# Performance work log

Measured on AMD Instinct MI355X. Metric: run time of the kernel, lower is better.

## Reference

```python
import jax, jax.numpy as jnp
import numpy as np

H, DK = 8, 64
INNER = H * DK  # 512


def rel_shift(x):
    # Transformer-XL relative shift (NeMo style): pad left, reshape, drop first row.
    b, h, q, p = x.shape
    x = jnp.pad(x, ((0, 0), (0, 0), (0, 0), (1, 0)))
    x = x.reshape(b, h, p + 1, q)[:, :, 1:]
    return x.reshape(b, h, q, p)


def setup_inputs() -> dict:
    key = jax.random.key(0)
    ks = jax.random.split(key, 16)
    B, T, D = 8, 1024, 512
    s_d = 1.0 / np.sqrt(D)
    s_i = 1.0 / np.sqrt(INNER)
    return {
        "x": jax.random.normal(ks[0], (B, T, D), jnp.float32),
        "pos_emb": jax.random.normal(ks[1], (1, 2 * T - 1, INNER), jnp.float32),
        "w_qkv": jax.random.normal(ks[2], (D, 3 * INNER), jnp.float32) * s_d,
        "w_q": jax.random.normal(ks[3], (INNER, INNER), jnp.float32) * s_i,
        "b_q": jnp.zeros((INNER,), jnp.float32),
        "w_k": jax.random.normal(ks[4], (INNER, INNER), jnp.float32) * s_i,
        "b_k": jnp.zeros((INNER,), jnp.float32),
        "w_v": jax.random.normal(ks[5], (INNER, INNER), jnp.float32) * s_i,
        "b_v": jnp.zeros((INNER,), jnp.float32),
        "w_pos": jax.random.normal(ks[6], (INNER, INNER), jnp.float32) * s_i,
        "bias_u": jax.random.normal(ks[7], (H, DK), jnp.float32) * 0.02,
        "bias_v": jax.random.normal(ks[8], (H, DK), jnp.float32) * 0.02,
        "w_ao": jax.random.normal(ks[9], (INNER, INNER), jnp.float32) * s_i,
        "b_ao": jnp.zeros((INNER,), jnp.float32),
        "w_o": jax.random.normal(ks[10], (INNER, D), jnp.float32) * s_i,
        "b_o": jnp.zeros((D,), jnp.float32),
    }


def reference(x, pos_emb, w_qkv, w_q, b_q, w_k, b_k, w_v, b_v, w_pos,
              bias_u, bias_v, w_ao, b_ao, w_o, b_o):
    B, T, D = x.shape
    # wrapper qkv projection (no bias), then chunk
    q, k, v = jnp.split(x @ w_qkv, 3, axis=-1)
    # RelPositionMultiHeadAttention internal projections
    q = (q @ w_q + b_q).reshape(B, T, H, DK)                       # (b,t,h,d)
    k = (k @ w_k + b_k).reshape(B, T, H, DK).transpose(0, 2, 1, 3)  # (b,h,t,d)
    v = (v @ w_v + b_v).reshape(B, T, H, DK).transpose(0, 2, 1, 3)  # (b,h,t,d)
    p = (pos_emb @ w_pos).reshape(pos_emb.shape[0], -1, H, DK).transpose(0, 2, 1, 3)  # (1,h,2t-1,d)
    q_u = (q + bias_u).transpose(0, 2, 1, 3)  # (b,h,t,d)
    q_v = (q + bias_v).transpose(0, 2, 1, 3)
    matrix_ac = jnp.einsum('bhqd,bhkd->bhqk', q_u, k)      # (b,h,t,t)
    matrix_bd = jnp.einsum('bhqd,xhpd->bhqp', q_v, p)      # (b,h,t,2t-1)
    matrix_bd = rel_shift(matrix_bd)[..., :T]
    scores = (matrix_ac + matrix_bd) * (1.0 / np.sqrt(DK))
    attn = jax.nn.softmax(scores, axis=-1)  # mask=None, dropout inactive at eval
    out = jnp.einsum('bhqk,bhkd->bhqd', attn, v)
    out = out.transpose(0, 2, 1, 3).reshape(B, T, INNER)
    out = out @ w_ao + b_ao   # attention linear_out
    return out @ w_o + b_o    # wrapper to_out
```

## Files before the change

### kernel.cpp

```cpp
#include <hip/hip_runtime.h>
#include <hip/hip_bf16.h>
#include <math.h>

#define H_     8
#define DK_    64
#define INNER_ 512
#define B_     8
#define T_     1024
#define D_     512
#define PLEN_  2047
#define BT_    8192

typedef __attribute__((ext_vector_type(8))) short bf16x8;
typedef __attribute__((ext_vector_type(4))) float f32x4;
typedef __attribute__((ext_vector_type(4))) unsigned short u16x4;
typedef __attribute__((ext_vector_type(8))) unsigned short u16x8;

__device__ __forceinline__ unsigned short f2bf(float f) {
    unsigned u = __float_as_uint(f);
    u += 0x7fffu + ((u >> 16) & 1u);
    return (unsigned short)(u >> 16);
}
__device__ __forceinline__ float bf2f(unsigned short s) {
    return __uint_as_float(((unsigned)s) << 16);
}
__device__ __forceinline__ f32x4 mfma16(bf16x8 a, bf16x8 b, f32x4 c) {
    return __builtin_amdgcn_mfma_f32_16x16x32_bf16(a, b, c, 0, 0, 0);
}
__device__ __forceinline__ void gload16(const unsigned short* g, unsigned short* l) {
    __builtin_amdgcn_global_load_lds(
        (const __attribute__((address_space(1))) void*)g,
        (__attribute__((address_space(3))) void*)l,
        16, 0, 0);
}
#define BARRIER()  __builtin_amdgcn_s_barrier()
#define SCHEDBAR() __builtin_amdgcn_sched_barrier(0)
#define VMCNT(N)   asm volatile("s_waitcnt vmcnt(" #N ")" ::: "memory")

#define QSCALE 0.125f

struct SplitA {
    const float* s[4];
    unsigned short* h[4];
    unsigned short* l[4];
    long n[4];
    int wantl[4];
};
__global__ __launch_bounds__(256) void split4(SplitA a)
{
    const int seg = blockIdx.y;
    long i4 = ((long)blockIdx.x * 256 + threadIdx.x) * 4;
    if (i4 >= a.n[seg]) return;
    f32x4 v = *(const f32x4*)(a.s[seg] + i4);
    u16x4 hh, ll;
    #pragma unroll
    for (int i = 0; i < 4; ++i) {
        unsigned short hb = f2bf(v[i]);
        hh[i] = hb;
        ll[i] = f2bf(v[i] - bf2f(hb));
    }
    *(u16x4*)(a.h[seg] + i4) = hh;
    if (a.wantl[seg]) *(u16x4*)(a.l[seg] + i4) = ll;
}

struct PrepW {
    const float* w[5];
    unsigned short* wh[5];
    unsigned short* wl[5];
};
__global__ __launch_bounds__(256) void prep_wb(PrepW p)
{
    const int z = blockIdx.z;
    const float* w = p.w[z];
    unsigned short* wh = p.wh[z];
    unsigned short* wl = p.wl[z];
    __shared__ float sW[32][36];
    const int t = threadIdx.x;
    const int n0 = blockIdx.x * 32, k0 = blockIdx.y * 32;
    {
        int kr = t >> 3, c4 = (t & 7) * 4;
        f32x4 v = *(const f32x4*)(w + (size_t)(k0 + kr) * 512 + n0 + c4);
        #pragma unroll
        for (int i = 0; i < 4; ++i) sW[kr][c4 + i] = v[i];
    }
    __syncthreads();
    {
        int nr = t >> 3, kc = (t & 7) * 4;
        u16x4 hv, lv;
        #pragma unroll
        for (int i = 0; i < 4; ++i) {
            float f = sW[kc + i][nr];
            unsigned short hb = f2bf(f);
            hv[i] = hb;
            lv[i] = f2bf(f - bf2f(hb));
        }
        *(u16x4*)(wh + (size_t)(n0 + nr) * 512 + k0 + kc) = hv;
        *(u16x4*)(wl + (size_t)(n0 + nr) * 512 + k0 + kc) = lv;
    }
}

__global__ __launch_bounds__(256) void misc_k(
    const float* __restrict__ b_ao, const float* __restrict__ w_o,
    const float* __restrict__ b_o, float* __restrict__ be,
    unsigned short* __restrict__ pb_base)
{
    if (blockIdx.x < 2) {
        int n = blockIdx.x * 256 + threadIdx.x;
        float s = b_o[n];
        for (int j = 0; j < 512; ++j) s += b_ao[j] * w_o[(size_t)j * 512 + n];
        be[n] = s;
    } else {
        ((unsigned int*)pb_base)[threadIdx.x] = 0u;
    }
}

template<int MF, bool ALO>
__device__ __forceinline__ void gemm_core(
    f32x4 (&acc)[MF][4],
    const unsigned short* __restrict__ Ah_g,
    const unsigned short* __restrict__ Al_g, int lda,
    const unsigned short* __restrict__ Wh_g,
    const unsigned short* __restrict__ Wl_g, int ldw,
    int M, int row0, int col0,
    unsigned short* sAh, unsigned short* sAl,
    unsigned short* sWh, unsigned short* sWl)
{
    const int t = threadIdx.x;
    const int lane = t & 63, w = t >> 6;
    const int wm = w >> 1, wn = w & 1;
    const int ln15 = lane & 15, g4 = lane >> 4;
    const int ASZ = MF * 32 * 32;
    const int WSZ = 128 * 32;
    constexpr int NLD = (MF / 2) * (ALO ? 2 : 1) + 4;

    auto stage = [&](int kt, int buf) {
        #pragma unroll
        for (int l = 0; l < MF / 2; ++l) {
            int e = l * 256 + w * 64 + lane;
            int row = e >> 2, slot = e & 3;
            int ss = slot ^ (row & 3);
            int gr = row0 + row;
            if (gr > M - 1) gr = M - 1;
            size_t ga = (size_t)gr * lda + kt * 32 + ss * 8;
            gload16(Ah_g + ga, sAh + buf * ASZ + (l * 256 + w * 64) * 8);
            if constexpr (ALO)
                gload16(Al_g + ga, sAl + buf * ASZ + (l * 256 + w * 64) * 8);
        }
        #pragma unroll
        for (int l = 0; l < 2; ++l) {
            int e = l * 256 + w * 64 + lane;
            int row = e >> 2, slot = e & 3;
            int ss = slot ^ (row & 3);
            size_t gw = (size_t)(col0 + row) * ldw + kt * 32 + ss * 8;
            gload16(Wh_g + gw, sWh + buf * WSZ + (l * 256 + w * 64) * 8);
            gload16(Wl_g + gw, sWl + buf * WSZ + (l * 256 + w * 64) * 8);
        }
    };
    auto comp = [&](int buf) {
        bf16x8 fah[MF], fal[MF], fwh[4], fwl[4];
        #pragma unroll
        for (int i = 0; i < MF; ++i) {
            int ar = wm * (MF * 16) + i * 16 + ln15;
            int sa = (g4 ^ (ar & 3)) * 8;
            fah[i] = *(const bf16x8*)&sAh[buf * ASZ + ar * 32 + sa];
            if constexpr (ALO)
                fal[i] = *(const bf16x8*)&sAl[buf * ASZ + ar * 32 + sa];
        }
        #pragma unroll
        for (int j = 0; j < 4; ++j) {
            int wr = wn * 64 + j * 16 + ln15;
            int sw = (g4 ^ (wr & 3)) * 8;
            fwh[j] = *(const bf16x8*)&sWh[buf * WSZ + wr * 32 + sw];
            fwl[j] = *(const bf16x8*)&sWl[buf * WSZ + wr * 32 + sw];
        }
        __builtin_amdgcn_s_setprio(1);
        #pragma unroll
        for (int mi = 0; mi < MF; ++mi)
            #pragma unroll
            for (int ni = 0; ni < 4; ++ni) {
                acc[mi][ni] = mfma16(fah[mi], fwh[ni], acc[mi][ni]);
                acc[mi][ni] = mfma16(fah[mi], fwl[ni], acc[mi][ni]);
                if constexpr (ALO)
                    acc[mi][ni] = mfma16(fal[mi], fwh[ni], acc[mi][ni]);
            }
        __builtin_amdgcn_s_setprio(0);
    };

    stage(0, 0);
    for (int k2 = 0; k2 < 8; ++k2) {
        BARRIER();
        stage(2 * k2 + 1, 1);
        if constexpr (NLD == 6) { VMCNT(6); } else { VMCNT(8); }
        BARRIER(); SCHEDBAR();
        comp(0);
        BARRIER();
        if (k2 < 7) {
            stage(2 * k2 + 2, 0);
            if constexpr (NLD == 6) { VMCNT(6); } else { VMCNT(8); }
        } else {
            VMCNT(0);
        }
        BARRIER(); SCHEDBAR();
        comp(1);
    }
}

#define GEMM_LDS3(MF) \
    __shared__ __align__(16) unsigned short sAh[2][MF * 32 * 32]; \
    __shared__ __align__(16) unsigned short sAl[2][MF * 32 * 32]; \
    __shared__ __align__(16) unsigned short sWh[2][128 * 32];     \
    __shared__ __align__(16) unsigned short sWl[2][128 * 32];
#define GEMM_LDS2(MF) \
    __shared__ __align__(16) unsigned short sAh[2][MF * 32 * 32]; \
    __shared__ __align__(16) unsigned short sWh[2][128 * 32];     \
    __shared__ __align__(16) unsigned short sWl[2][128 * 32];

__global__ __launch_bounds__(256, 3) void gemm_qkvp(
    const unsigned short* __restrict__ Ah_g,
    const unsigned short* __restrict__ Wh_g,
    const unsigned short* __restrict__ Wl_g,
    const unsigned short* __restrict__ posh,
    const unsigned short* __restrict__ wp_h,
    const unsigned short* __restrict__ wp_l,
    const float* __restrict__ b_q, const float* __restrict__ bu,
    const float* __restrict__ bv, const float* __restrict__ b_k,
    const float* __restrict__ b_v,
    unsigned short* __restrict__ qu, unsigned short* __restrict__ qv,
    unsigned short* __restrict__ kb, unsigned short* __restrict__ vt,
    unsigned short* __restrict__ pb0)
{
    GEMM_LDS2(4)
    f32x4 acc[4][4];
    #pragma unroll
    for (int i = 0; i < 4; ++i)
        #pragma unroll
        for (int j = 0; j < 4; ++j) acc[i][j] = (f32x4){0.f, 0.f, 0.f, 0.f};

    const int bx = blockIdx.x, by = blockIdx.y;
    const bool isPos = (bx == 12);
    int row0, col0, M;
    const unsigned short *Ag, *Whg, *Wlg;
    if (isPos) {
        row0 = (by >> 2) * 128; col0 = (by & 3) * 128;
        Ag = posh; Whg = wp_h; Wlg = wp_l; M = PLEN_;
    } else {
        row0 = by * 128; col0 = bx * 128;
        Ag = Ah_g; Whg = Wh_g; Wlg = Wl_g; M = BT_;
    }
    gemm_core<4, false>(acc, Ag, nullptr, 512, Whg, Wlg, 512, M, row0, col0,
                        &sAh[0][0], &sAh[0][0], &sWh[0][0], &sWl[0][0]);

    const int t = threadIdx.x;
    const int lane = t & 63, w = t >> 6;
    const int wm = w >> 1, wn = w & 1;
    const int ln15 = lane & 15, g4 = lane >> 4;

    if (isPos) {
        #pragma unroll
        for (int mi = 0; mi < 4; ++mi)
            #pragma unroll
            for (int r4 = 0; r4 < 4; ++r4) {
                int gr = row0 + wm * 64 + mi * 16 + g4 * 4 + r4;
                if (gr >= PLEN_) continue;
                #pragma unroll
                for (int ni = 0; ni < 4; ++ni) {
                    int gc = col0 + wn * 64 + ni * 16 + ln15;
                    pb0[(size_t)gr * 512 + gc] = f2bf(acc[mi][ni][r4]);
                }
            }
        return;
    }

    const int grp = col0 >> 9;
    if (grp == 2) {
        #pragma unroll
        for (int mi = 0; mi < 4; ++mi) {
            int gr0 = row0 + wm * 64 + mi * 16 + g4 * 4;
            int bb = gr0 >> 10, t0 = gr0 & 1023;
            #pragma unroll
            for (int ni = 0; ni < 4; ++ni) {
                int gcl = (col0 & 511) + wn * 64 + ni * 16 + ln15;
                float bias = b_v[gcl];
                u16x4 vv;
                #pragma unroll
                for (int r4 = 0; r4 < 4; ++r4) vv[r4] = f2bf(acc[mi][ni][r4] + bias);
                *(u16x4*)(vt + ((size_t)(bb * 512 + gcl)) * 1024 + t0) = vv;
            }
        }
    } else {
        #pragma unroll
        for (int mi = 0; mi < 4; ++mi)
            #pragma unroll
            for (int r4 = 0; r4 < 4; ++r4) {
                int gr = row0 + wm * 64 + mi * 16 + g4 * 4 + r4;
                #pragma unroll
                for (int ni = 0; ni < 4; ++ni) {
                    int gcl = (col0 & 511) + wn * 64 + ni * 16 + ln15;
                    float a = acc[mi][ni][r4];
                    if (grp == 0) {
                        float base = a + b_q[gcl];
                        qu[(size_t)gr * 512 + gcl] = f2bf((base + bu[gcl]) * QSCALE);
                        qv[(size_t)gr * 512 + gcl] = f2bf((base + bv[gcl]) * QSCALE);
                    } else {
                        kb[(size_t)gr * 512 + gcl] = f2bf(a + b_k[gcl]);
                    }
                }
            }
    }
}

struct WeffT {
    const unsigned short* ah[4];
    const unsigned short* al[4];
    const unsigned short* wh[4];
    const unsigned short* wl[4];
    int ldw[4];
    unsigned short* ch[4];
    unsigned short* cl[4];
};
__global__ __launch_bounds__(256, 3) void gemm_wefft(WeffT a)
{
    GEMM_LDS3(2)
    const int z = blockIdx.z;
    f32x4 acc[2][4];
    #pragma unroll
    for (int i = 0; i < 2; ++i)
        #pragma unroll
        for (int j = 0; j < 4; ++j) acc[i][j] = (f32x4){0.f, 0.f, 0.f, 0.f};
    const int row0 = blockIdx.y * 64, col0 = blockIdx.x * 128;
    gemm_core<2, true>(acc, a.ah[z], a.al[z], 512, a.wh[z], a.wl[z], a.ldw[z],
                       512, row0, col0,
                       &sAh[0][0], &sAl[0][0], &sWh[0][0], &sWl[0][0]);

    const int t = threadIdx.x;
    const int lane = t & 63, w = t >> 6;
    const int wm = w >> 1, wn = w & 1;
    const int ln15 = lane & 15, g4 = lane >> 4;
    unsigned short* Ch = a.ch[z];
    unsigned short* Cl = a.cl[z];
    #pragma unroll
    for (int mi = 0; mi < 2; ++mi)
        #pragma unroll
        for (int r4 = 0; r4 < 4; ++r4) {
            int gr = row0 + wm * 32 + mi * 16 + g4 * 4 + r4;
            #pragma unroll
            for (int ni = 0; ni < 4; ++ni) {
                int gc = col0 + wn * 64 + ni * 16 + ln15;
                float v = acc[mi][ni][r4];
                unsigned short hb = f2bf(v);
                Ch[(size_t)gr * 512 + gc] = hb;
                Cl[(size_t)gr * 512 + gc] = f2bf(v - bf2f(hb));
            }
        }
}

__global__ __launch_bounds__(256, 3) void gemm_out(
    const unsigned short* __restrict__ Ah_g,
    const unsigned short* __restrict__ Al_g,
    const unsigned short* __restrict__ Wh_g,
    const unsigned short* __restrict__ Wl_g,
    const float* __restrict__ beff, float* __restrict__ C)
{
    GEMM_LDS3(2)
    f32x4 acc[2][4];
    #pragma unroll
    for (int i = 0; i < 2; ++i)
        #pragma unroll
        for (int j = 0; j < 4; ++j) acc[i][j] = (f32x4){0.f, 0.f, 0.f, 0.f};
    const int row0 = blockIdx.y * 64, col0 = blockIdx.x * 128;
    gemm_core<2, true>(acc, Ah_g, Al_g, 512, Wh_g, Wl_g, 512, BT_, row0, col0,
                       &sAh[0][0], &sAl[0][0], &sWh[0][0], &sWl[0][0]);

    const int t = threadIdx.x;
    const int lane = t & 63, w = t >> 6;
    const int wm = w >> 1, wn = w & 1;
    const int ln15 = lane & 15, g4 = lane >> 4;
    #pragma unroll
    for (int mi = 0; mi < 2; ++mi)
        #pragma unroll
        for (int r4 = 0; r4 < 4; ++r4) {
            int gr = row0 + wm * 32 + mi * 16 + g4 * 4 + r4;
            #pragma unroll
            for (int ni = 0; ni < 4; ++ni) {
                int gc = col0 + wn * 64 + ni * 16 + ln15;
                C[(size_t)gr * 512 + gc] = acc[mi][ni][r4] + beff[gc];
            }
        }
}

__global__ __launch_bounds__(256, 2) void attn_v12(
    const unsigned short* __restrict__ qu_g,
    const unsigned short* __restrict__ qv_g,
    const unsigned short* __restrict__ kb_g,
    const unsigned short* __restrict__ vt_g,
    const unsigned short* __restrict__ pb_g,
    unsigned short* __restrict__ atth,
    unsigned short* __restrict__ attl)
{
    __shared__ __align__(16) unsigned short sK[2][64 * 64];
    __shared__ __align__(16) unsigned short sP[2][64 * 64];
    __shared__ __align__(16) unsigned short sV[2][64 * 64];
    __shared__ __align__(16) unsigned short ringb[64][132];
    __shared__ __align__(16) unsigned short sProb[64][72];

    const int t = threadIdx.x;
    const int lane = t & 63, w = t >> 6;
    const int ln15 = lane & 15, g4 = lane >> 4;

    const int wg = blockIdx.x;
    const int idx = (wg & 7) * 128 + (wg >> 3);
    const int q0 = (idx & 15) * 64;
    const int bh = idx >> 4;
    const int h = bh & 7, b = bh >> 3;
    const size_t tok0 = (size_t)b * T_;
    const int hd = h * DK_;
    const int qq = w * 16 + ln15;

    auto stage_chunk = [&](int c, int buf) {
        #pragma unroll
        for (int l = 0; l < 2; ++l) {
            int e = l * 256 + w * 64 + lane;
            int row = e >> 3, slot = e & 7;
            int sl = slot ^ (row & 7);
            int lofs = buf * 4096 + (l * 256 + w * 64) * 8;
            gload16(kb_g + (tok0 + c * 64 + row) * INNER_ + hd + sl * 8, &sK[0][lofs]);
            gload16(vt_g + ((size_t)(b * H_ + h) * DK_ + row) * T_ + c * 64 + sl * 8, &sV[0][lofs]);
            long p = (long)(c * 64 - q0 + 1023 + row);
            gload16(pb_g + p * INNER_ + hd + sl * 8, &sP[0][lofs]);
        }
    };

    #pragma unroll
    for (int l = 0; l < 2; ++l) {
        int e = l * 256 + w * 64 + lane;
        int row = e >> 3, slot = e & 7;
        int sl = slot ^ (row & 7);
        size_t src = (tok0 + q0 + row) * INNER_ + hd + sl * 8;
        gload16(qu_g + src, &sK[0][(l * 256 + w * 64) * 8]);
        gload16(qv_g + src, &sP[0][(l * 256 + w * 64) * 8]);
    }
    __syncthreads();
    bf16x8 fqu[2], fqv[2];
    #pragma unroll
    for (int ki = 0; ki < 2; ++ki) {
        int sl = (ki * 4 + g4) ^ (qq & 7);
        fqu[ki] = *(const bf16x8*)&sK[0][qq * 64 + sl * 8];
        fqv[ki] = *(const bf16x8*)&sP[0][qq * 64 + sl * 8];
    }
    __syncthreads();

    #pragma unroll
    for (int l = 0; l < 2; ++l) {
        int e = l * 256 + w * 64 + lane;
        int row = e >> 3, slot = e & 7;
        int sl = slot ^ (row & 7);
        long p = (long)(959 - q0 + row);
        gload16(pb_g + p * INNER_ + hd + sl * 8, &sP[0][4096 + (l * 256 + w * 64) * 8]);
    }
    stage_chunk(0, 0);
    __syncthreads();

    #pragma unroll
    for (int n = 0; n < 4; ++n) {
        f32x4 bdv = {0.f, 0.f, 0.f, 0.f};
        #pragma unroll
        for (int ki = 0; ki < 2; ++ki) {
            int prow = n * 16 + ln15;
            int sl = (ki * 4 + g4) ^ (prow & 7);
            bf16x8 pf = *(const bf16x8*)&sP[0][4096 + prow * 64 + sl * 8];
            bdv = mfma16(pf, fqv[ki], bdv);
        }
        #pragma unroll
        for (int r4 = 0; r4 < 4; ++r4)
            ringb[qq][(n * 16 + g4 * 4 + r4 + qq) & 127] = f2bf(bdv[r4]);
    }
    __syncthreads();

    float m = -1e30f, den = 0.f;
    f32x4 o[4];
    #pragma unroll
    for (int i = 0; i < 4; ++i) o[i] = (f32x4){0.f, 0.f, 0.f, 0.f};

    auto compute_chunk = [&](int c, int buf) {
        const int bofs = buf * 4096;
        f32x4 sc[4], bd[4];
        #pragma unroll
        for (int n = 0; n < 4; ++n) {
            sc[n] = (f32x4){0.f, 0.f, 0.f, 0.f};
            bd[n] = (f32x4){0.f, 0.f, 0.f, 0.f};
        }
        __builtin_amdgcn_s_setprio(1);
        #pragma unroll
        for (int ki = 0; ki < 2; ++ki)
            #pragma unroll
            for (int n = 0; n < 4; ++n) {
                int krow = n * 16 + ln15;
                int sl = (ki * 4 + g4) ^ (krow & 7);
                bf16x8 kf = *(const bf16x8*)&sK[0][bofs + krow * 64 + sl * 8];
                sc[n] = mfma16(kf, fqu[ki], sc[n]);
                bf16x8 pf = *(const bf16x8*)&sP[0][bofs + krow * 64 + sl * 8];
                bd[n] = mfma16(pf, fqv[ki], bd[n]);
            }
        __builtin_amdgcn_s_setprio(0);

        const int pbase = (c & 1) ? 0 : 64;
        #pragma unroll
        for (int n = 0; n < 4; ++n)
            #pragma unroll
            for (int r4 = 0; r4 < 4; ++r4)
                ringb[qq][(pbase + n * 16 + g4 * 4 + r4 + qq) & 127] = f2bf(bd[n][r4]);

        float s[4][4];
        float mx = -1e30f;
        #pragma unroll
        for (int n = 0; n < 4; ++n) {
            const int st2 = (c * 64 + 64 + n * 16 + g4 * 4) & 127;
            u16x4 rv = *(const u16x4*)&ringb[qq][st2];
            #pragma unroll
            for (int r4 = 0; r4 < 4; ++r4) {
                float v = sc[n][r4] + bf2f(rv[r4]);
                s[n][r4] = v;
                mx = fmaxf(mx, v);
            }
        }
        mx = fmaxf(mx, __shfl_xor(mx, 16));
        mx = fmaxf(mx, __shfl_xor(mx, 32));
        float newm = fmaxf(m, mx);
        float scale = __expf(m - newm);
        m = newm;
        float ls = 0.f;
        #pragma unroll
        for (int n = 0; n < 4; ++n) {
            u16x4 pv4;
            #pragma unroll
            for (int r4 = 0; r4 < 4; ++r4) {
                float p = __expf(s[n][r4] - newm);
                ls += p;
                pv4[r4] = f2bf(p);
            }
            *(u16x4*)&sProb[qq][n * 16 + g4 * 4] = pv4;
        }
        ls += __shfl_xor(ls, 16);
        ls += __shfl_xor(ls, 32);
        den = den * scale + ls;
        #pragma unroll
        for (int n2 = 0; n2 < 4; ++n2) {
            o[n2][0] *= scale; o[n2][1] *= scale;
            o[n2][2] *= scale; o[n2][3] *= scale;
        }

        __builtin_amdgcn_s_setprio(1);
        #pragma unroll
        for (int ki = 0; ki < 2; ++ki) {
            bf16x8 pa = *(const bf16x8*)&sProb[qq][ki * 32 + g4 * 8];
            #pragma unroll
            for (int n2 = 0; n2 < 4; ++n2) {
                int drow = n2 * 16 + ln15;
                int sl = (ki * 4 + g4) ^ (drow & 7);
                bf16x8 vf = *(const bf16x8*)&sV[0][bofs + drow * 64 + sl * 8];
                o[n2] = mfma16(vf, pa, o[n2]);
            }
        }
        __builtin_amdgcn_s_setprio(0);
    };

    for (int c2 = 0; c2 < 8; ++c2) {
        int c = c2 * 2;
        stage_chunk(c + 1, 1);
        compute_chunk(c, 0);
        __syncthreads();
        if (c2 < 7) stage_chunk(c + 2, 0);
        compute_chunk(c + 1, 1);
        __syncthreads();
    }

    const float inv = 1.0f / den;
    #pragma unroll
    for (int n2 = 0; n2 < 4; ++n2) {
        u16x4 hv, lv;
        #pragma unroll
        for (int r4 = 0; r4 < 4; ++r4) {
            float val = o[n2][r4] * inv;
            unsigned short hb = f2bf(val);
            hv[r4] = hb;
            lv[r4] = f2bf(val - bf2f(hb));
        }
        size_t oidx = (tok0 + q0 + qq) * INNER_ + hd + n2 * 16 + g4 * 4;
        *(u16x4*)(atth + oidx) = hv;
        *(u16x4*)(attl + oidx) = lv;
    }
}

extern "C" void kernel_launch(void* const* d_in, const int* in_sizes, int n_in,
                              void* d_out, int out_size, void* d_ws, size_t ws_size,
                              hipStream_t stream)
{
    const float* x     = (const float*)d_in[0];
    const float* pos   = (const float*)d_in[1];
    const float* w_qkv = (const float*)d_in[2];
    const float* w_q   = (const float*)d_in[3];
    const float* b_q   = (const float*)d_in[4];
    const float* w_k   = (const float*)d_in[5];
    const float* b_k   = (const float*)d_in[6];
    const float* w_v   = (const float*)d_in[7];
    const float* b_v   = (const float*)d_in[8];
    const float* w_pos = (const float*)d_in[9];
    const float* bu    = (const float*)d_in[10];
    const float* bv    = (const float*)d_in[11];
    const float* w_ao  = (const float*)d_in[12];
    const float* b_ao  = (const float*)d_in[13];
    const float* w_o   = (const float*)d_in[14];
    const float* b_o   = (const float*)d_in[15];
    float* out = (float*)d_out;

    unsigned short* u = (unsigned short*)d_ws;
    const size_t SZ = (size_t)BT_ * INNER_;
    unsigned short* xh   = u;
    unsigned short* xl   = xh + SZ;
    unsigned short* qu   = xl + SZ;
    unsigned short* qv   = qu + SZ;
    unsigned short* kb   = qv + SZ;
    unsigned short* vt   = kb + SZ;
    unsigned short* atth = vt + SZ;
    unsigned short* attl = atth + SZ;
    unsigned short* pb_base = attl + SZ;
    unsigned short* pb0  = pb_base + 512;
    unsigned short* posh = pb_base + 1049600;
    unsigned short* posl = posh + 1049600;
    unsigned short* wqkvh = posl + 1049600;
    unsigned short* wqkvl = wqkvh + 786432;
    unsigned short* waoh  = wqkvl + 786432;
    unsigned short* waol  = waoh + 262144;
    unsigned short* w5    = waol + 262144;
    unsigned short* wq_h = w5;              unsigned short* wq_l = w5 + 262144;
    unsigned short* wk_h = w5 + 2*262144;   unsigned short* wk_l = w5 + 3*262144;
    unsigned short* wv_h = w5 + 4*262144;   unsigned short* wv_l = w5 + 5*262144;
    unsigned short* wo_h = w5 + 6*262144;   unsigned short* wo_l = w5 + 7*262144;
    unsigned short* wp_h = w5 + 8*262144;   unsigned short* wp_l = w5 + 9*262144;
    unsigned short* wcat_h = w5 + 10*262144;
    unsigned short* wcat_l = wcat_h + 786432;
    unsigned short* woe_h  = wcat_l + 786432;
    unsigned short* woe_l  = woe_h + 262144;
    float* beff = (float*)(woe_l + 262144);

    dim3 blk(256);

    SplitA sa;
    sa.s[0] = x;     sa.h[0] = xh;    sa.l[0] = xl;    sa.n[0] = (long)SZ;          sa.wantl[0] = 0;
    sa.s[1] = w_qkv; sa.h[1] = wqkvh; sa.l[1] = wqkvl; sa.n[1] = 786432L;           sa.wantl[1] = 1;
    sa.s[2] = w_ao;  sa.h[2] = waoh;  sa.l[2] = waol;  sa.n[2] = 262144L;           sa.wantl[2] = 1;
    sa.s[3] = pos;   sa.h[3] = posh;  sa.l[3] = posl;  sa.n[3] = (long)PLEN_ * 512; sa.wantl[3] = 0;
    split4<<<dim3(4096, 4), blk, 0, stream>>>(sa);

    PrepW p5;
    p5.w[0] = w_q;   p5.wh[0] = wq_h; p5.wl[0] = wq_l;
    p5.w[1] = w_k;   p5.wh[1] = wk_h; p5.wl[1] = wk_l;
    p5.w[2] = w_v;   p5.wh[2] = wv_h; p5.wl[2] = wv_l;
    p5.w[3] = w_o;   p5.wh[3] = wo_h; p5.wl[3] = wo_l;
    p5.w[4] = w_pos; p5.wh[4] = wp_h; p5.wl[4] = wp_l;
    prep_wb<<<dim3(16, 16, 5), blk, 0, stream>>>(p5);

    WeffT wt;
    wt.ah[0] = wq_h; wt.al[0] = wq_l;
    wt.ah[1] = wk_h; wt.al[1] = wk_l;
    wt.ah[2] = wv_h; wt.al[2] = wv_l;
    wt.ah[3] = wo_h; wt.al[3] = wo_l;
    wt.wh[0] = wqkvh;        wt.wl[0] = wqkvl;        wt.ldw[0] = 1536;
    wt.wh[1] = wqkvh + 512;  wt.wl[1] = wqkvl + 512;  wt.ldw[1] = 1536;
    wt.wh[2] = wqkvh + 1024; wt.wl[2] = wqkvl + 1024; wt.ldw[2] = 1536;
    wt.wh[3] = waoh;         wt.wl[3] = waol;         wt.ldw[3] = 512;
    wt.ch[0] = wcat_h;            wt.cl[0] = wcat_l;
    wt.ch[1] = wcat_h + 262144;   wt.cl[1] = wcat_l + 262144;
    wt.ch[2] = wcat_h + 2*262144; wt.cl[2] = wcat_l + 2*262144;
    wt.ch[3] = woe_h;             wt.cl[3] = woe_l;
    gemm_wefft<<<dim3(4, 8, 4), blk, 0, stream>>>(wt);

    misc_k<<<3, blk, 0, stream>>>(b_ao, w_o, b_o, beff, pb_base);

    gemm_qkvp<<<dim3(13, 64), blk, 0, stream>>>(xh, wcat_h, wcat_l,
        posh, wp_h, wp_l,
        b_q, bu, bv, b_k, b_v, qu, qv, kb, vt, pb0);

    attn_v12<<<1024, blk, 0, stream>>>(qu, qv, kb, vt, pb0, atth, attl);

    gemm_out<<<dim3(4, 128), blk, 0, stream>>>(atth, attl, woe_h, woe_l, beff, out);
}
```

Before: 185.6 us.

## Drop low-bf16 attention output split and merge prep kernels into one launch

The attention kernel now writes only the high bf16 part of its output, and the output GEMM drops the A-low MFMA term and its LDS buffer. This cuts global writes, reads and a third of the MFMAs in the final GEMM. The three preprocessing kernels (split, weight transpose-split, bias/misc) are merged into a single launch to save launch overhead. In exchange, accuracy drops because the attention output is kept only to bf16 precision.

```diff
diff --git a/kernel.cpp b/kernel.cpp
--- a/kernel.cpp
+++ b/kernel.cpp
@@ -39,78 +39,77 @@
 
 #define QSCALE 0.125f
 
-struct SplitA {
+struct PrepAll {
     const float* s[4];
     unsigned short* h[4];
     unsigned short* l[4];
     long n[4];
     int wantl[4];
-};
-__global__ __launch_bounds__(256) void split4(SplitA a)
-{
-    const int seg = blockIdx.y;
-    long i4 = ((long)blockIdx.x * 256 + threadIdx.x) * 4;
-    if (i4 >= a.n[seg]) return;
-    f32x4 v = *(const f32x4*)(a.s[seg] + i4);
-    u16x4 hh, ll;
-    #pragma unroll
-    for (int i = 0; i < 4; ++i) {
-        unsigned short hb = f2bf(v[i]);
-        hh[i] = hb;
-        ll[i] = f2bf(v[i] - bf2f(hb));
-    }
-    *(u16x4*)(a.h[seg] + i4) = hh;
-    if (a.wantl[seg]) *(u16x4*)(a.l[seg] + i4) = ll;
-}
-
-struct PrepW {
     const float* w[5];
     unsigned short* wh[5];
     unsigned short* wl[5];
+    const float* b_ao;
+    const float* w_o;
+    const float* b_o;
+    float* be;
+    unsigned short* pb_base;
 };
-__global__ __launch_bounds__(256) void prep_wb(PrepW p)
+__global__ __launch_bounds__(256) void prep_all(PrepAll a)
 {
-    const int z = blockIdx.z;
-    const float* w = p.w[z];
-    unsigned short* wh = p.wh[z];
-    unsigned short* wl = p.wl[z];
-    __shared__ float sW[32][36];
+    const int y = blockIdx.y;
     const int t = threadIdx.x;
-    const int n0 = blockIdx.x * 32, k0 = blockIdx.y * 32;
-    {
-        int kr = t >> 3, c4 = (t & 7) * 4;
-        f32x4 v = *(const f32x4*)(w + (size_t)(k0 + kr) * 512 + n0 + c4);
-        #pragma unroll
-        for (int i = 0; i < 4; ++i) sW[kr][c4 + i] = v[i];
-    }
-    __syncthreads();
-    {
-        int nr = t >> 3, kc = (t & 7) * 4;
-        u16x4 hv, lv;
+    if (y < 4) {
+        long i4 = ((long)blockIdx.x * 256 + t) * 4;
+        if (i4 >= a.n[y]) return;
+        f32x4 v = *(const f32x4*)(a.s[y] + i4);
+        u16x4 hh, ll;
         #pragma unroll
         for (int i = 0; i < 4; ++i) {
-            float f = sW[kc + i][nr];
-            unsigned short hb = f2bf(f);
-            hv[i] = hb;
-            lv[i] = f2bf(f - bf2f(hb));
-        }
-        *(u16x4*)(wh + (size_t)(n0 + nr) * 512 + k0 + kc) = hv;
-        *(u16x4*)(wl + (size_t)(n0 + nr) * 512 + k0 + kc) = lv;
-    }
-}
-
-__global__ __launch_bounds__(256) void misc_k(
-    const float* __restrict__ b_ao, const float* __restrict__ w_o,
-    const float* __restrict__ b_o, float* __restrict__ be,
-    unsigned short* __restrict__ pb_base)
-{
-    if (blockIdx.x < 2) {
-        int n = blockIdx.x * 256 + threadIdx.x;
-        float s = b_o[n];
-        for (int j = 0; j < 512; ++j) s += b_ao[j] * w_o[(size_t)j * 512 + n];
-        be[n] = s;
-    } else {
-        ((unsigned int*)pb_base)[threadIdx.x] = 0u;
+            unsigned short hb = f2bf(v[i]);
+            hh[i] = hb;
+            ll[i] = f2bf(v[i] - bf2f(hb));
+        }
+        *(u16x4*)(a.h[y] + i4) = hh;
+        if (a.wantl[y]) *(u16x4*)(a.l[y] + i4) = ll;
+        return;
+    }
+    const int x = blockIdx.x;
+    if (x < 1280) {
+        __shared__ float sW[32][36];
+        const int z = x >> 8, idx = x & 255;
+        const int n0 = (idx & 15) * 32, k0 = (idx >> 4) * 32;
+        const float* w = a.w[z];
+        unsigned short* wh = a.wh[z];
+        unsigned short* wl = a.wl[z];
+        {
+            int kr = t >> 3, c4 = (t & 7) * 4;
+            f32x4 v = *(const f32x4*)(w + (size_t)(k0 + kr) * 512 + n0 + c4);
+            #pragma unroll
+            for (int i = 0; i < 4; ++i) sW[kr][c4 + i] = v[i];
+        }
+        __syncthreads();
+        {
+            int nr = t >> 3, kc = (t & 7) * 4;
+            u16x4 hv, lv;
+            #pragma unroll
+            for (int i = 0; i < 4; ++i) {
+                float f = sW[kc + i][nr];
+                unsigned short hb = f2bf(f);
+                hv[i] = hb;
+                lv[i] = f2bf(f - bf2f(hb));
+            }
+            *(u16x4*)(wh + (size_t)(n0 + nr) * 512 + k0 + kc) = hv;
+            *(u16x4*)(wl + (size_t)(n0 + nr) * 512 + k0 + kc) = lv;
+        }
+        return;
+    }
+    if (x < 1282) {
+        int n = (x - 1280) * 256 + t;
+        float s = a.b_o[n];
+        for (int j = 0; j < 512; ++j) s += a.b_ao[j] * a.w_o[(size_t)j * 512 + n];
+        a.be[n] = s;
+    } else if (x == 1282) {
+        ((unsigned int*)a.pb_base)[t] = 0u;
     }
 }
 
@@ -190,13 +189,17 @@
     for (int k2 = 0; k2 < 8; ++k2) {
         BARRIER();
         stage(2 * k2 + 1, 1);
-        if constexpr (NLD == 6) { VMCNT(6); } else { VMCNT(8); }
+        if constexpr (NLD == 6) { VMCNT(6); }
+        else if constexpr (NLD == 5) { VMCNT(5); }
+        else { VMCNT(8); }
         BARRIER(); SCHEDBAR();
         comp(0);
         BARRIER();
         if (k2 < 7) {
             stage(2 * k2 + 2, 0);
-            if constexpr (NLD == 6) { VMCNT(6); } else { VMCNT(8); }
+            if constexpr (NLD == 6) { VMCNT(6); }
+            else if constexpr (NLD == 5) { VMCNT(5); }
+            else { VMCNT(8); }
         } else {
             VMCNT(0);
         }
@@ -356,20 +359,19 @@
 
 __global__ __launch_bounds__(256, 3) void gemm_out(
     const unsigned short* __restrict__ Ah_g,
-    const unsigned short* __restrict__ Al_g,
     const unsigned short* __restrict__ Wh_g,
     const unsigned short* __restrict__ Wl_g,
     const float* __restrict__ beff, float* __restrict__ C)
 {
-    GEMM_LDS3(2)
+    GEMM_LDS2(2)
     f32x4 acc[2][4];
     #pragma unroll
     for (int i = 0; i < 2; ++i)
         #pragma unroll
         for (int j = 0; j < 4; ++j) acc[i][j] = (f32x4){0.f, 0.f, 0.f, 0.f};
     const int row0 = blockIdx.y * 64, col0 = blockIdx.x * 128;
-    gemm_core<2, true>(acc, Ah_g, Al_g, 512, Wh_g, Wl_g, 512, BT_, row0, col0,
-                       &sAh[0][0], &sAl[0][0], &sWh[0][0], &sWl[0][0]);
+    gemm_core<2, false>(acc, Ah_g, nullptr, 512, Wh_g, Wl_g, 512, BT_, row0, col0,
+                        &sAh[0][0], &sAh[0][0], &sWh[0][0], &sWl[0][0]);
 
     const int t = threadIdx.x;
     const int lane = t & 63, w = t >> 6;
@@ -388,14 +390,13 @@
         }
 }
 
-__global__ __launch_bounds__(256, 2) void attn_v12(
+__global__ __launch_bounds__(256, 2) void attn_v14(
     const unsigned short* __restrict__ qu_g,
     const unsigned short* __restrict__ qv_g,
     const unsigned short* __restrict__ kb_g,
     const unsigned short* __restrict__ vt_g,
     const unsigned short* __restrict__ pb_g,
-    unsigned short* __restrict__ atth,
-    unsigned short* __restrict__ attl)
+    unsigned short* __restrict__ atth)
 {
     __shared__ __align__(16) unsigned short sK[2][64 * 64];
     __shared__ __align__(16) unsigned short sP[2][64 * 64];
@@ -577,17 +578,12 @@
     const float inv = 1.0f / den;
     #pragma unroll
     for (int n2 = 0; n2 < 4; ++n2) {
-        u16x4 hv, lv;
-        #pragma unroll
-        for (int r4 = 0; r4 < 4; ++r4) {
-            float val = o[n2][r4] * inv;
-            unsigned short hb = f2bf(val);
-            hv[r4] = hb;
-            lv[r4] = f2bf(val - bf2f(hb));
-        }
+        u16x4 hv;
+        #pragma unroll
+        for (int r4 = 0; r4 < 4; ++r4)
+            hv[r4] = f2bf(o[n2][r4] * inv);
         size_t oidx = (tok0 + q0 + qq) * INNER_ + hd + n2 * 16 + g4 * 4;
         *(u16x4*)(atth + oidx) = hv;
-        *(u16x4*)(attl + oidx) = lv;
     }
 }
 
@@ -645,20 +641,18 @@
 
     dim3 blk(256);
 
-    SplitA sa;
-    sa.s[0] = x;     sa.h[0] = xh;    sa.l[0] = xl;    sa.n[0] = (long)SZ;          sa.wantl[0] = 0;
-    sa.s[1] = w_qkv; sa.h[1] = wqkvh; sa.l[1] = wqkvl; sa.n[1] = 786432L;           sa.wantl[1] = 1;
-    sa.s[2] = w_ao;  sa.h[2] = waoh;  sa.l[2] = waol;  sa.n[2] = 262144L;           sa.wantl[2] = 1;
-    sa.s[3] = pos;   sa.h[3] = posh;  sa.l[3] = posl;  sa.n[3] = (long)PLEN_ * 512; sa.wantl[3] = 0;
-    split4<<<dim3(4096, 4), blk, 0, stream>>>(sa);
-
-    PrepW p5;
-    p5.w[0] = w_q;   p5.wh[0] = wq_h; p5.wl[0] = wq_l;
-    p5.w[1] = w_k;   p5.wh[1] = wk_h; p5.wl[1] = wk_l;
-    p5.w[2] = w_v;   p5.wh[2] = wv_h; p5.wl[2] = wv_l;
-    p5.w[3] = w_o;   p5.wh[3] = wo_h; p5.wl[3] = wo_l;
-    p5.w[4] = w_pos; p5.wh[4] = wp_h; p5.wl[4] = wp_l;
-    prep_wb<<<dim3(16, 16, 5), blk, 0, stream>>>(p5);
+    PrepAll pa;
+    pa.s[0] = x;     pa.h[0] = xh;    pa.l[0] = xl;    pa.n[0] = (long)SZ;          pa.wantl[0] = 0;
+    pa.s[1] = w_qkv; pa.h[1] = wqkvh; pa.l[1] = wqkvl; pa.n[1] = 786432L;           pa.wantl[1] = 1;
+    pa.s[2] = w_ao;  pa.h[2] = waoh;  pa.l[2] = waol;  pa.n[2] = 262144L;           pa.wantl[2] = 1;
+    pa.s[3] = pos;   pa.h[3] = posh;  pa.l[3] = posl;  pa.n[3] = (long)PLEN_ * 512; pa.wantl[3] = 0;
+    pa.w[0] = w_q;   pa.wh[0] = wq_h; pa.wl[0] = wq_l;
+    pa.w[1] = w_k;   pa.wh[1] = wk_h; pa.wl[1] = wk_l;
+    pa.w[2] = w_v;   pa.wh[2] = wv_h; pa.wl[2] = wv_l;
+    pa.w[3] = w_o;   pa.wh[3] = wo_h; pa.wl[3] = wo_l;
+    pa.w[4] = w_pos; pa.wh[4] = wp_h; pa.wl[4] = wp_l;
+    pa.b_ao = b_ao; pa.w_o = w_o; pa.b_o = b_o; pa.be = beff; pa.pb_base = pb_base;
+    prep_all<<<dim3(4096, 5), blk, 0, stream>>>(pa);
 
     WeffT wt;
     wt.ah[0] = wq_h; wt.al[0] = wq_l;
@@ -675,13 +669,11 @@
     wt.ch[3] = woe_h;             wt.cl[3] = woe_l;
     gemm_wefft<<<dim3(4, 8, 4), blk, 0, stream>>>(wt);
 
-    misc_k<<<3, blk, 0, stream>>>(b_ao, w_o, b_o, beff, pb_base);
-
     gemm_qkvp<<<dim3(13, 64), blk, 0, stream>>>(xh, wcat_h, wcat_l,
         posh, wp_h, wp_l,
         b_q, bu, bv, b_k, b_v, qu, qv, kb, vt, pb0);
 
-    attn_v12<<<1024, blk, 0, stream>>>(qu, qv, kb, vt, pb0, atth, attl);
-
-    gemm_out<<<dim3(4, 128), blk, 0, stream>>>(atth, attl, woe_h, woe_l, beff, out);
-}
+    attn_v14<<<1024, blk, 0, stream>>>(qu, qv, kb, vt, pb0, atth);
+
+    gemm_out<<<dim3(4, 128), blk, 0, stream>>>(atth, woe_h, woe_l, beff, out);
+}
```

New measurement: 175.0 us. -5.7%, faster.
